# Optimization experiments

Measured on AMD Instinct MI355X. Metric: run time of the kernel, lower is better.

## Reference

```python
import jax, jax.numpy as jnp
import numpy as np
import math

C = 1.0
IN_FEATURES = 512
SCALE = 1.0 / math.sqrt(IN_FEATURES)  # 1/sqrt(input_size) * lr_mul, lr_mul=1
LR_MUL = 1.0
GAIN = math.sqrt(2.0)
EPS = 1e-5       # clamp epsilon used by hyptorch-style pmath
PROJ_EPS = 1e-3  # boundary epsilon for project()


def _norm(x):
    return jnp.linalg.norm(x, axis=-1, keepdims=True)


def _artanh(x):
    return jnp.arctanh(jnp.clip(x, -1.0 + EPS, 1.0 - EPS))


def _project(x, c):
    sqrt_c = c ** 0.5
    norm = jnp.maximum(_norm(x), EPS)
    maxnorm = (1.0 - PROJ_EPS) / sqrt_c
    return jnp.where(norm > maxnorm, x / norm * maxnorm, x)


def _expmap0(u, c):
    sqrt_c = c ** 0.5
    u_norm = jnp.maximum(_norm(u), EPS)
    return jnp.tanh(sqrt_c * u_norm) * u / (sqrt_c * u_norm)


def _mobius_add(x, y, c):
    x2 = jnp.sum(x * x, axis=-1, keepdims=True)
    y2 = jnp.sum(y * y, axis=-1, keepdims=True)
    xy = jnp.sum(x * y, axis=-1, keepdims=True)
    num = (1.0 + 2.0 * c * xy + c * y2) * x + (1.0 - c * x2) * y
    denom = 1.0 + 2.0 * c * xy + c * c * x2 * y2
    return num / (denom + EPS)


def _mobius_matvec(m, x, c):
    # m: [out, in], x: [N, in]
    sqrt_c = c ** 0.5
    x_norm = jnp.maximum(_norm(x), EPS)
    mx = x @ m.T  # [N, out]
    mx_norm = jnp.maximum(_norm(mx), EPS)
    res = jnp.tanh(mx_norm / x_norm * _artanh(sqrt_c * x_norm)) * mx / (mx_norm * sqrt_c)
    zero_row = jnp.all(mx == 0, axis=-1, keepdims=True)
    return jnp.where(zero_row, jnp.zeros_like(res), res)


def _mobius_scalar_mult(x, r, c):
    sqrt_c = c ** 0.5
    x_norm = jnp.maximum(_norm(x), EPS)
    return jnp.tanh(r * _artanh(sqrt_c * x_norm)) * x / (x_norm * sqrt_c)


def setup_inputs() -> dict:
    key = jax.random.key(0)
    k1, k2, k3 = jax.random.split(key, 3)
    N, D_IN, D_OUT = 131072, 512, 512
    # scale x so points lie well inside the unit Poincare ball (norm ~ 0.45)
    x = jax.random.normal(k1, (N, D_IN), dtype=jnp.float32) * 0.02
    weight = jax.random.normal(k2, (D_OUT, D_IN), dtype=jnp.float32)
    bias = jax.random.normal(k3, (D_OUT,), dtype=jnp.float32) * 0.01
    return {"x": x, "weight": weight, "bias": bias}


def reference(x, weight, bias):
    c = C
    mv = _mobius_matvec(weight * SCALE, x, c)
    b = _expmap0(bias * LR_MUL, c)
    out = _project(_mobius_add(mv, b[None, :], c), c)
    out = jax.nn.leaky_relu(out, 0.2)
    out = _mobius_scalar_mult(out, GAIN, c)
    return out
```

## Files before the change

kernel.cpp:

```cpp
#include <hip/hip_runtime.h>
#include <math.h>

#define EPSV 1e-5f
#define SCALE_W 0.0441941738241592f
#define GAIN_R 1.4142135623730951f

typedef __attribute__((ext_vector_type(8))) short bf16x8;
typedef __attribute__((ext_vector_type(4))) float f32x4;

static __device__ __forceinline__ unsigned short f2bf(float f) {
  union { float f; unsigned int u; } v; v.f = f;
  unsigned int r = v.u + 0x7FFFu + ((v.u >> 16) & 1u);
  return (unsigned short)(r >> 16);
}

#define LBAR() do {                                          \
  asm volatile("s_waitcnt lgkmcnt(0)" ::: "memory");         \
  __builtin_amdgcn_sched_barrier(0);                         \
  __builtin_amdgcn_s_barrier();                              \
  __builtin_amdgcn_sched_barrier(0);                         \
  asm volatile("" ::: "memory");                             \
} while (0)

__global__ void bias_expmap_k(const float* __restrict__ bias, float* __restrict__ bexp,
                              float* __restrict__ y2out) {
  __shared__ float part[8];
  int t = threadIdx.x;
  float bv = bias[t];
  float s = bv * bv;
  s += __shfl_xor(s, 1);  s += __shfl_xor(s, 2);  s += __shfl_xor(s, 4);
  s += __shfl_xor(s, 8);  s += __shfl_xor(s, 16); s += __shfl_xor(s, 32);
  if ((t & 63) == 0) part[t >> 6] = s;
  __syncthreads();
  float tot = 0.f;
#pragma unroll
  for (int i = 0; i < 8; ++i) tot += part[i];
  float un = fmaxf(sqrtf(tot), EPSV);
  float th = tanhf(un);
  bexp[t] = th * bv / un;
  if (t == 0) *y2out = th * th;
}

__global__ void pack_weight_k(const float* __restrict__ w, unsigned short* __restrict__ wsB) {
  int e = blockIdx.x * 256 + threadIdx.x;
  int o = e >> 9;
  int k = e & 511;
  int ks = k >> 5, kk = k & 31;
  int lgr = kk >> 3, j = kk & 7;
  int colhi = o >> 4, l15 = o & 15;
  int dst = ((ks * 32 + colhi) * 64 + lgr * 16 + l15) * 8 + j;
  wsB[dst] = f2bf(w[e] * SCALE_W);
}

#define RB 80
#define KSROW 5120
#define BUFSZ 20480
#define SC_OFF 40960
#define SMEMSZ 43776

__global__ __launch_bounds__(256, 2)
void hyp_main_k(const float* __restrict__ x, const unsigned short* __restrict__ wsB,
                const float* __restrict__ bexp, const float* __restrict__ y2p,
                float* __restrict__ out, int tilesPerBlk) {
  extern __shared__ char smem[];
  const int tid  = threadIdx.x;
  const int lane = tid & 63;
  const int wave = tid >> 6;
  const int l15  = lane & 15;
  const int lgr  = lane >> 4;
  const int srow = tid >> 2;
  const int sq   = tid & 3;

  float* xn2 = (float*)(smem + SC_OFF);
  float* pS2 = (float*)(smem + SC_OFF + 256);
  float* pSB = (float*)(smem + SC_OFF + 1280);
  float* g12 = (float*)(smem + SC_OFF + 2304);

  const char* ard0 = smem + l15 * RB + lgr * 16;
  const char* brd  = (const char*)wsB + ((size_t)(wave * 8) * 64 + lane) * 16;
  char* awr0 = smem + sq * KSROW + srow * RB;

  f32x4 acc[4][8];
#pragma unroll
  for (int mf = 0; mf < 4; ++mf)
#pragma unroll
    for (int nf = 0; nf < 8; ++nf) acc[mf][nf] = f32x4{0.f, 0.f, 0.f, 0.f};

  const long base = (long)blockIdx.x * tilesPerBlk;
  const int nss = 4 * tilesPerBlk;
  float xss = 0.f;
  f32x4 st[8];

  {
    const float* p = x + (size_t)(base * 64 + srow) * 512 + sq * 32;
#pragma unroll
    for (int i = 0; i < 8; ++i) st[i] = *(const f32x4*)(p + i * 4);
#pragma unroll
    for (int i = 0; i < 8; ++i) {
      f32x4 v = st[i];
      xss += v[0] * v[0] + v[1] * v[1] + v[2] * v[2] + v[3] * v[3];
      uint2 pk;
      pk.x = (unsigned int)f2bf(v[0]) | ((unsigned int)f2bf(v[1]) << 16);
      pk.y = (unsigned int)f2bf(v[2]) | ((unsigned int)f2bf(v[3]) << 16);
      *(uint2*)(awr0 + i * 8) = pk;
    }
  }
  LBAR();

  for (int s = 0; s < nss; ++s) {
    const int q = s & 3;
    const int buf = s & 1;

    if (s + 1 < nss) {
      const int sp = s + 1;
      const float* p = x + (size_t)((base + (sp >> 2)) * 64 + srow) * 512 + (sp & 3) * 128 + sq * 32;
#pragma unroll
      for (int i = 0; i < 8; ++i) st[i] = *(const f32x4*)(p + i * 4);
    }

#pragma unroll
    for (int ksl = 0; ksl < 4; ++ksl) {
      const int gks = q * 4 + ksl;
      bf16x8 xf[4], wf[8];
#pragma unroll
      for (int mf = 0; mf < 4; ++mf)
        xf[mf] = *(const bf16x8*)(ard0 + buf * BUFSZ + ksl * KSROW + mf * 1280);
#pragma unroll
      for (int nf = 0; nf < 8; ++nf)
        wf[nf] = *(const bf16x8*)(brd + (size_t)gks * 32768 + nf * 1024);
#pragma unroll
      for (int mf = 0; mf < 4; ++mf)
#pragma unroll
        for (int nf = 0; nf < 8; ++nf)
          acc[mf][nf] = __builtin_amdgcn_mfma_f32_16x16x32_bf16(wf[nf], xf[mf], acc[mf][nf], 0, 0, 0);
    }

    if (q == 3) {
      const long tile = base + (s >> 2);

      float xs = xss;
      xs += __shfl_xor(xs, 1); xs += __shfl_xor(xs, 2);
      if (sq == 0) xn2[srow] = xs;
      xss = 0.f;

      f32x4 bvv[8];
#pragma unroll
      for (int nf = 0; nf < 8; ++nf)
        bvv[nf] = *(const f32x4*)(bexp + wave * 128 + nf * 16 + lgr * 4);

      float s2[4], sb[4];
#pragma unroll
      for (int mf = 0; mf < 4; ++mf) {
        s2[mf] = 0.f; sb[mf] = 0.f;
#pragma unroll
        for (int nf = 0; nf < 8; ++nf)
#pragma unroll
          for (int j = 0; j < 4; ++j) {
            float v = acc[mf][nf][j];
            s2[mf] += v * v;
            sb[mf] += v * bvv[nf][j];
          }
        s2[mf] += __shfl_xor(s2[mf], 16); s2[mf] += __shfl_xor(s2[mf], 32);
        sb[mf] += __shfl_xor(sb[mf], 16); sb[mf] += __shfl_xor(sb[mf], 32);
      }
      if (lane < 16) {
#pragma unroll
        for (int mf = 0; mf < 4; ++mf) {
          pS2[(mf * 16 + l15) * 4 + wave] = s2[mf];
          pSB[(mf * 16 + l15) * 4 + wave] = sb[mf];
        }
      }
      LBAR();

      if (tid < 64) {
        int r = tid;
        float S2 = 0.f, SB = 0.f;
#pragma unroll
        for (int i = 0; i < 4; ++i) { S2 += pS2[r * 4 + i]; SB += pSB[r * 4 + i]; }
        float y2 = *y2p;
        float xn  = fmaxf(sqrtf(xn2[r]), EPSV);
        float mxn = fmaxf(sqrtf(S2), EPSV);
        float f = tanhf((mxn / xn) * atanhf(fminf(xn, 1.f - EPSV))) / mxn;
        float xy = f * SB;
        float x2 = f * f * S2;
        float den = 1.f + 2.f * xy + x2 * y2 + EPSV;
        float g1 = (1.f + 2.f * xy + y2) * f / den;
        float g2 = (1.f - x2) / den;
        float n1sq = g1 * g1 * S2 + 2.f * g1 * g2 * SB + g2 * g2 * y2;
        float n1 = fmaxf(sqrtf(fmaxf(n1sq, 0.f)), EPSV);
        if (n1 > 0.999f) { float sc = 0.999f / n1; g1 *= sc; g2 *= sc; }
        g12[r * 2] = g1; g12[r * 2 + 1] = g2;
      }
      LBAR();

      float n2p[4];
#pragma unroll
      for (int mf = 0; mf < 4; ++mf) {
        float g1 = g12[(mf * 16 + l15) * 2], g2 = g12[(mf * 16 + l15) * 2 + 1];
        n2p[mf] = 0.f;
#pragma unroll
        for (int nf = 0; nf < 8; ++nf)
#pragma unroll
          for (int j = 0; j < 4; ++j) {
            float v = g1 * acc[mf][nf][j] + g2 * bvv[nf][j];
            v = v > 0.f ? v : 0.2f * v;
            acc[mf][nf][j] = v;
            n2p[mf] += v * v;
          }
        n2p[mf] += __shfl_xor(n2p[mf], 16); n2p[mf] += __shfl_xor(n2p[mf], 32);
      }
      if (lane < 16) {
#pragma unroll
        for (int mf = 0; mf < 4; ++mf) pS2[(mf * 16 + l15) * 4 + wave] = n2p[mf];
      }
      LBAR();

      if (tid < 64) {
        int r = tid;
        float sn = 0.f;
#pragma unroll
        for (int i = 0; i < 4; ++i) sn += pS2[r * 4 + i];
        float n2 = fmaxf(sqrtf(sn), EPSV);
        xn2[r] = tanhf(GAIN_R * atanhf(fminf(n2, 1.f - EPSV))) / n2;
      }
      LBAR();

#pragma unroll
      for (int mf = 0; mf < 4; ++mf) {
        float tm = xn2[mf * 16 + l15];
#pragma unroll
        for (int nf = 0; nf < 8; ++nf) {
          f32x4 o = acc[mf][nf];
          o[0] *= tm; o[1] *= tm; o[2] *= tm; o[3] *= tm;
          *(f32x4*)(out + (size_t)(tile * 64 + mf * 16 + l15) * 512 +
                    wave * 128 + nf * 16 + lgr * 4) = o;
          acc[mf][nf] = f32x4{0.f, 0.f, 0.f, 0.f};
        }
      }
    }

    if (s + 1 < nss) {
      char* awr = awr0 + ((s + 1) & 1) * BUFSZ;
#pragma unroll
      for (int i = 0; i < 8; ++i) {
        f32x4 v = st[i];
        xss += v[0] * v[0] + v[1] * v[1] + v[2] * v[2] + v[3] * v[3];
        uint2 pk;
        pk.x = (unsigned int)f2bf(v[0]) | ((unsigned int)f2bf(v[1]) << 16);
        pk.y = (unsigned int)f2bf(v[2]) | ((unsigned int)f2bf(v[3]) << 16);
        *(uint2*)(awr + i * 8) = pk;
      }
    }
    LBAR();
  }
}

extern "C" void kernel_launch(void* const* d_in, const int* in_sizes, int n_in,
                              void* d_out, int out_size, void* d_ws, size_t ws_size,
                              hipStream_t stream) {
  const float* x    = (const float*)d_in[0];
  const float* w    = (const float*)d_in[1];
  const float* bias = (const float*)d_in[2];
  float* out = (float*)d_out;

  unsigned short* wsB = (unsigned short*)d_ws;
  float* bexp = (float*)((char*)d_ws + 524288);
  float* y2p  = (float*)((char*)d_ws + 524288 + 2048);

  bias_expmap_k<<<dim3(1), dim3(512), 0, stream>>>(bias, bexp, y2p);
  pack_weight_k<<<dim3(1024), dim3(256), 0, stream>>>(w, wsB);

  const int nrows  = in_sizes[0] / 512;
  const int ntiles = nrows / 64;
  const int nblk   = 512;
  const int tpb    = ntiles / nblk;
  hyp_main_k<<<dim3(nblk), dim3(256), SMEMSZ, stream>>>(x, wsB, bexp, y2p, out, tpb);
}
```

Before: 177.7 us.

## Stream weights through LDS via global_load_lds with deeper x prefetch and 8 waves

Restructures the main GEMM loop to process one 32-wide K-slice per iteration. Weight slices are staged into double-buffered LDS with direct global-to-LDS loads, replacing per-wave global weight reads. The x operand is prefetched two slices ahead into a 4-slot LDS ring. Blocks grow to 512 threads (8 waves, each owning 64 output columns), the grid is halved, and bias values are hoisted out of the epilogue. The intent is better latency hiding and less redundant weight traffic, at the cost of more barriers per K step, higher LDS usage, and fragile vmcnt-based wait accounting.

```diff
diff --git a/kernel.cpp b/kernel.cpp
--- a/kernel.cpp
+++ b/kernel.cpp
@@ -13,13 +13,21 @@
   unsigned int r = v.u + 0x7FFFu + ((v.u >> 16) & 1u);
   return (unsigned short)(r >> 16);
 }
+
+#define GLD_LDS16(gsrc, ldst)                                                                      \
+  __builtin_amdgcn_global_load_lds((const __attribute__((address_space(1))) unsigned int*)(gsrc),  \
+                                   (__attribute__((address_space(3))) unsigned int*)(ldst), 16, 0, 0)
 
 #define LBAR() do {                                          \
   asm volatile("s_waitcnt lgkmcnt(0)" ::: "memory");         \
   __builtin_amdgcn_sched_barrier(0);                         \
   __builtin_amdgcn_s_barrier();                              \
   __builtin_amdgcn_sched_barrier(0);                         \
-  asm volatile("" ::: "memory");                             \
+} while (0)
+
+#define VMW5() do {                                          \
+  asm volatile("s_waitcnt vmcnt(5)" ::: "memory");           \
+  __builtin_amdgcn_sched_barrier(0);                         \
 } while (0)
 
 __global__ void bias_expmap_k(const float* __restrict__ bias, float* __restrict__ bexp,
@@ -52,13 +60,12 @@
   wsB[dst] = f2bf(w[e] * SCALE_W);
 }
 
-#define RB 80
-#define KSROW 5120
-#define BUFSZ 20480
-#define SC_OFF 40960
-#define SMEMSZ 43776
-
-__global__ __launch_bounds__(256, 2)
+#define ASLOT 4608
+#define BOFF_L 18432
+#define SCR 83968
+#define SMEMSZ 88832
+
+__global__ __launch_bounds__(512, 2)
 void hyp_main_k(const float* __restrict__ x, const unsigned short* __restrict__ wsB,
                 const float* __restrict__ bexp, const float* __restrict__ y2p,
                 float* __restrict__ out, int tilesPerBlk) {
@@ -68,92 +75,99 @@
   const int wave = tid >> 6;
   const int l15  = lane & 15;
   const int lgr  = lane >> 4;
-  const int srow = tid >> 2;
-  const int sq   = tid & 3;
-
-  float* xn2 = (float*)(smem + SC_OFF);
-  float* pS2 = (float*)(smem + SC_OFF + 256);
-  float* pSB = (float*)(smem + SC_OFF + 1280);
-  float* g12 = (float*)(smem + SC_OFF + 2304);
-
-  const char* ard0 = smem + l15 * RB + lgr * 16;
-  const char* brd  = (const char*)wsB + ((size_t)(wave * 8) * 64 + lane) * 16;
-  char* awr0 = smem + sq * KSROW + srow * RB;
-
-  f32x4 acc[4][8];
+  const int arow = tid >> 3;
+  const int ag   = tid & 7;
+
+  float* xn2 = (float*)(smem + SCR);
+  float* pS2 = (float*)(smem + SCR + 256);
+  float* pSB = (float*)(smem + SCR + 2304);
+  float* g12 = (float*)(smem + SCR + 4352);
+
+  f32x4 bvv[4];
+#pragma unroll
+  for (int nf = 0; nf < 4; ++nf)
+    bvv[nf] = *(const f32x4*)(bexp + wave * 64 + nf * 16 + lgr * 4);
+  float y2v = *y2p;
+
+  f32x4 acc[4][4];
 #pragma unroll
   for (int mf = 0; mf < 4; ++mf)
 #pragma unroll
-    for (int nf = 0; nf < 8; ++nf) acc[mf][nf] = f32x4{0.f, 0.f, 0.f, 0.f};
-
-  const long base = (long)blockIdx.x * tilesPerBlk;
-  const int nss = 4 * tilesPerBlk;
+    for (int nf = 0; nf < 4; ++nf) acc[mf][nf] = f32x4{0.f, 0.f, 0.f, 0.f};
+
+  const long tile0 = (long)blockIdx.x * tilesPerBlk;
+  const int U = tilesPerBlk * 16;
+  const float* xbase = x + (size_t)(tile0 * 64 + arow) * 512 + ag * 4;
+
   float xss = 0.f;
-  f32x4 st[8];
+  f32x4 Lprev, Lcur;
 
   {
-    const float* p = x + (size_t)(base * 64 + srow) * 512 + sq * 32;
-#pragma unroll
-    for (int i = 0; i < 8; ++i) st[i] = *(const f32x4*)(p + i * 4);
-#pragma unroll
-    for (int i = 0; i < 8; ++i) {
-      f32x4 v = st[i];
+    f32x4 a0 = *(const f32x4*)(xbase);
+    f32x4 a1 = *(const f32x4*)(xbase + 32);
+#pragma unroll
+    for (int i = 0; i < 2; ++i) {
+      f32x4 v = (i == 0) ? a0 : a1;
       xss += v[0] * v[0] + v[1] * v[1] + v[2] * v[2] + v[3] * v[3];
       uint2 pk;
       pk.x = (unsigned int)f2bf(v[0]) | ((unsigned int)f2bf(v[1]) << 16);
       pk.y = (unsigned int)f2bf(v[2]) | ((unsigned int)f2bf(v[3]) << 16);
-      *(uint2*)(awr0 + i * 8) = pk;
+      *(uint2*)(smem + i * ASLOT + arow * 72 + ag * 8) = pk;
     }
   }
+#pragma unroll
+  for (int r = 0; r < 4; ++r)
+    GLD_LDS16((const char*)wsB + r * 8192 + wave * 1024 + lane * 16,
+              smem + BOFF_L + r * 8192 + wave * 1024);
   LBAR();
 
-  for (int s = 0; s < nss; ++s) {
-    const int q = s & 3;
-    const int buf = s & 1;
-
-    if (s + 1 < nss) {
-      const int sp = s + 1;
-      const float* p = x + (size_t)((base + (sp >> 2)) * 64 + srow) * 512 + (sp & 3) * 128 + sq * 32;
-#pragma unroll
-      for (int i = 0; i < 8; ++i) st[i] = *(const f32x4*)(p + i * 4);
-    }
-
-#pragma unroll
-    for (int ksl = 0; ksl < 4; ++ksl) {
-      const int gks = q * 4 + ksl;
-      bf16x8 xf[4], wf[8];
+#pragma unroll 1
+  for (int u = 0; u < U; ++u) {
+    {
+      int gu = u + 2; if (gu >= U) gu = 0;
+      Lcur = *(const f32x4*)(xbase + (size_t)(gu >> 4) * 32768 + (gu & 15) * 32);
+    }
+    {
+      const char* bsrc = (const char*)wsB + (size_t)((u + 1) & 15) * 32768;
+      char* bdst = smem + BOFF_L + ((u + 1) & 1) * 32768;
+#pragma unroll
+      for (int r = 0; r < 4; ++r)
+        GLD_LDS16(bsrc + r * 8192 + wave * 1024 + lane * 16, bdst + r * 8192 + wave * 1024);
+    }
+    VMW5();
+    LBAR();
+
+    {
+      const char* as = smem + (u & 3) * ASLOT + l15 * 72 + lgr * 16;
+      const char* bb = smem + BOFF_L + (u & 1) * 32768 + (size_t)(wave * 4) * 1024 + lane * 16;
+      bf16x8 xf[4], wf[4];
+#pragma unroll
+      for (int mf = 0; mf < 4; ++mf) xf[mf] = *(const bf16x8*)(as + mf * (16 * 72));
+#pragma unroll
+      for (int nf = 0; nf < 4; ++nf) wf[nf] = *(const bf16x8*)(bb + nf * 1024);
+      __builtin_amdgcn_s_setprio(1);
 #pragma unroll
       for (int mf = 0; mf < 4; ++mf)
-        xf[mf] = *(const bf16x8*)(ard0 + buf * BUFSZ + ksl * KSROW + mf * 1280);
-#pragma unroll
-      for (int nf = 0; nf < 8; ++nf)
-        wf[nf] = *(const bf16x8*)(brd + (size_t)gks * 32768 + nf * 1024);
-#pragma unroll
-      for (int mf = 0; mf < 4; ++mf)
-#pragma unroll
-        for (int nf = 0; nf < 8; ++nf)
+#pragma unroll
+        for (int nf = 0; nf < 4; ++nf)
           acc[mf][nf] = __builtin_amdgcn_mfma_f32_16x16x32_bf16(wf[nf], xf[mf], acc[mf][nf], 0, 0, 0);
-    }
-
-    if (q == 3) {
-      const long tile = base + (s >> 2);
+      __builtin_amdgcn_s_setprio(0);
+    }
+
+    if ((u & 15) == 15) {
+      const long trow = (tile0 + (u >> 4)) * 64;
 
       float xs = xss;
-      xs += __shfl_xor(xs, 1); xs += __shfl_xor(xs, 2);
-      if (sq == 0) xn2[srow] = xs;
+      xs += __shfl_xor(xs, 1); xs += __shfl_xor(xs, 2); xs += __shfl_xor(xs, 4);
+      if ((lane & 7) == 0) xn2[wave * 8 + (lane >> 3)] = xs;
       xss = 0.f;
-
-      f32x4 bvv[8];
-#pragma unroll
-      for (int nf = 0; nf < 8; ++nf)
-        bvv[nf] = *(const f32x4*)(bexp + wave * 128 + nf * 16 + lgr * 4);
 
       float s2[4], sb[4];
 #pragma unroll
       for (int mf = 0; mf < 4; ++mf) {
         s2[mf] = 0.f; sb[mf] = 0.f;
 #pragma unroll
-        for (int nf = 0; nf < 8; ++nf)
+        for (int nf = 0; nf < 4; ++nf)
 #pragma unroll
           for (int j = 0; j < 4; ++j) {
             float v = acc[mf][nf][j];
@@ -166,8 +180,8 @@
       if (lane < 16) {
 #pragma unroll
         for (int mf = 0; mf < 4; ++mf) {
-          pS2[(mf * 16 + l15) * 4 + wave] = s2[mf];
-          pSB[(mf * 16 + l15) * 4 + wave] = sb[mf];
+          pS2[(mf * 16 + l15) * 8 + wave] = s2[mf];
+          pSB[(mf * 16 + l15) * 8 + wave] = sb[mf];
         }
       }
       LBAR();
@@ -176,17 +190,16 @@
         int r = tid;
         float S2 = 0.f, SB = 0.f;
 #pragma unroll
-        for (int i = 0; i < 4; ++i) { S2 += pS2[r * 4 + i]; SB += pSB[r * 4 + i]; }
-        float y2 = *y2p;
+        for (int i = 0; i < 8; ++i) { S2 += pS2[r * 8 + i]; SB += pSB[r * 8 + i]; }
         float xn  = fmaxf(sqrtf(xn2[r]), EPSV);
         float mxn = fmaxf(sqrtf(S2), EPSV);
         float f = tanhf((mxn / xn) * atanhf(fminf(xn, 1.f - EPSV))) / mxn;
         float xy = f * SB;
         float x2 = f * f * S2;
-        float den = 1.f + 2.f * xy + x2 * y2 + EPSV;
-        float g1 = (1.f + 2.f * xy + y2) * f / den;
+        float den = 1.f + 2.f * xy + x2 * y2v + EPSV;
+        float g1 = (1.f + 2.f * xy + y2v) * f / den;
         float g2 = (1.f - x2) / den;
-        float n1sq = g1 * g1 * S2 + 2.f * g1 * g2 * SB + g2 * g2 * y2;
+        float n1sq = g1 * g1 * S2 + 2.f * g1 * g2 * SB + g2 * g2 * y2v;
         float n1 = fmaxf(sqrtf(fmaxf(n1sq, 0.f)), EPSV);
         if (n1 > 0.999f) { float sc = 0.999f / n1; g1 *= sc; g2 *= sc; }
         g12[r * 2] = g1; g12[r * 2 + 1] = g2;
@@ -199,7 +212,7 @@
         float g1 = g12[(mf * 16 + l15) * 2], g2 = g12[(mf * 16 + l15) * 2 + 1];
         n2p[mf] = 0.f;
 #pragma unroll
-        for (int nf = 0; nf < 8; ++nf)
+        for (int nf = 0; nf < 4; ++nf)
 #pragma unroll
           for (int j = 0; j < 4; ++j) {
             float v = g1 * acc[mf][nf][j] + g2 * bvv[nf][j];
@@ -211,7 +224,7 @@
       }
       if (lane < 16) {
 #pragma unroll
-        for (int mf = 0; mf < 4; ++mf) pS2[(mf * 16 + l15) * 4 + wave] = n2p[mf];
+        for (int mf = 0; mf < 4; ++mf) pS2[(mf * 16 + l15) * 8 + wave] = n2p[mf];
       }
       LBAR();
 
@@ -219,7 +232,7 @@
         int r = tid;
         float sn = 0.f;
 #pragma unroll
-        for (int i = 0; i < 4; ++i) sn += pS2[r * 4 + i];
+        for (int i = 0; i < 8; ++i) sn += pS2[r * 8 + i];
         float n2 = fmaxf(sqrtf(sn), EPSV);
         xn2[r] = tanhf(GAIN_R * atanhf(fminf(n2, 1.f - EPSV))) / n2;
       }
@@ -229,28 +242,25 @@
       for (int mf = 0; mf < 4; ++mf) {
         float tm = xn2[mf * 16 + l15];
 #pragma unroll
-        for (int nf = 0; nf < 8; ++nf) {
+        for (int nf = 0; nf < 4; ++nf) {
           f32x4 o = acc[mf][nf];
           o[0] *= tm; o[1] *= tm; o[2] *= tm; o[3] *= tm;
-          *(f32x4*)(out + (size_t)(tile * 64 + mf * 16 + l15) * 512 +
-                    wave * 128 + nf * 16 + lgr * 4) = o;
+          *(f32x4*)(out + (size_t)(trow + mf * 16 + l15) * 512 +
+                    wave * 64 + nf * 16 + lgr * 4) = o;
           acc[mf][nf] = f32x4{0.f, 0.f, 0.f, 0.f};
         }
       }
     }
 
-    if (s + 1 < nss) {
-      char* awr = awr0 + ((s + 1) & 1) * BUFSZ;
-#pragma unroll
-      for (int i = 0; i < 8; ++i) {
-        f32x4 v = st[i];
-        xss += v[0] * v[0] + v[1] * v[1] + v[2] * v[2] + v[3] * v[3];
-        uint2 pk;
-        pk.x = (unsigned int)f2bf(v[0]) | ((unsigned int)f2bf(v[1]) << 16);
-        pk.y = (unsigned int)f2bf(v[2]) | ((unsigned int)f2bf(v[3]) << 16);
-        *(uint2*)(awr + i * 8) = pk;
-      }
-    }
+    if (u > 0) {
+      f32x4 v = Lprev;
+      xss += v[0] * v[0] + v[1] * v[1] + v[2] * v[2] + v[3] * v[3];
+      uint2 pk;
+      pk.x = (unsigned int)f2bf(v[0]) | ((unsigned int)f2bf(v[1]) << 16);
+      pk.y = (unsigned int)f2bf(v[2]) | ((unsigned int)f2bf(v[3]) << 16);
+      *(uint2*)(smem + ((u + 1) & 3) * ASLOT + arow * 72 + ag * 8) = pk;
+    }
+    Lprev = Lcur;
     LBAR();
   }
 }
@@ -272,7 +282,7 @@
 
   const int nrows  = in_sizes[0] / 512;
   const int ntiles = nrows / 64;
-  const int nblk   = 512;
+  const int nblk   = 256;
   const int tpb    = ntiles / nblk;
-  hyp_main_k<<<dim3(nblk), dim3(256), SMEMSZ, stream>>>(x, wsB, bexp, y2p, out, tpb);
-}
+  hyp_main_k<<<dim3(nblk), dim3(512), SMEMSZ, stream>>>(x, wsB, bexp, y2p, out, tpb);
+}
```

Result: slower. 264.4 us (+48.8%).

## Stream weight slices into LDS via async global_load_lds with per-k-step double buffering

Applied to the files above, without the earlier changes.

The main loop is restructured so each iteration handles one 32-wide k-slice instead of four. The weight slice is loaded asynchronously into double-buffered LDS with global_load_lds, where before each wave read weights straight from global memory. The next x slice is prefetched into registers, and explicit vmcnt waits control how far loads may run ahead. Bias and y2 are also cached in LDS and MFMA issue gets a raised priority. In exchange LDS use nearly doubles, which may limit occupancy, and there are now sixteen barriers per tile instead of four.

```diff
diff --git a/kernel.cpp b/kernel.cpp
--- a/kernel.cpp
+++ b/kernel.cpp
@@ -7,19 +7,28 @@
 
 typedef __attribute__((ext_vector_type(8))) short bf16x8;
 typedef __attribute__((ext_vector_type(4))) float f32x4;
+typedef __attribute__((ext_vector_type(4))) unsigned int u32x4;
 
 static __device__ __forceinline__ unsigned short f2bf(float f) {
   union { float f; unsigned int u; } v; v.f = f;
   unsigned int r = v.u + 0x7FFFu + ((v.u >> 16) & 1u);
   return (unsigned short)(r >> 16);
 }
+
+#define GLD_LDS16(gsrc, ldst)                                                                      \
+  __builtin_amdgcn_global_load_lds((const __attribute__((address_space(1))) unsigned int*)(gsrc),  \
+                                   (__attribute__((address_space(3))) unsigned int*)(ldst), 16, 0, 0)
 
 #define LBAR() do {                                          \
   asm volatile("s_waitcnt lgkmcnt(0)" ::: "memory");         \
   __builtin_amdgcn_sched_barrier(0);                         \
   __builtin_amdgcn_s_barrier();                              \
   __builtin_amdgcn_sched_barrier(0);                         \
-  asm volatile("" ::: "memory");                             \
+} while (0)
+
+#define VMCNT(N) do {                                        \
+  asm volatile("s_waitcnt vmcnt(" #N ")" ::: "memory");      \
+  __builtin_amdgcn_sched_barrier(0);                         \
 } while (0)
 
 __global__ void bias_expmap_k(const float* __restrict__ bias, float* __restrict__ bexp,
@@ -53,10 +62,11 @@
 }
 
 #define RB 80
-#define KSROW 5120
-#define BUFSZ 20480
-#define SC_OFF 40960
-#define SMEMSZ 43776
+#define ABUF 5120
+#define BOFF 10240
+#define BBUF 32768
+#define SCR 75776
+#define SMEMSZ 80896
 
 __global__ __launch_bounds__(256, 2)
 void hyp_main_k(const float* __restrict__ x, const unsigned short* __restrict__ wsB,
@@ -71,14 +81,12 @@
   const int srow = tid >> 2;
   const int sq   = tid & 3;
 
-  float* xn2 = (float*)(smem + SC_OFF);
-  float* pS2 = (float*)(smem + SC_OFF + 256);
-  float* pSB = (float*)(smem + SC_OFF + 1280);
-  float* g12 = (float*)(smem + SC_OFF + 2304);
-
-  const char* ard0 = smem + l15 * RB + lgr * 16;
-  const char* brd  = (const char*)wsB + ((size_t)(wave * 8) * 64 + lane) * 16;
-  char* awr0 = smem + sq * KSROW + srow * RB;
+  float* xn2      = (float*)(smem + SCR);
+  float* pS2      = (float*)(smem + SCR + 256);
+  float* pSB      = (float*)(smem + SCR + 1280);
+  float* g12      = (float*)(smem + SCR + 2304);
+  float* bexp_lds = (float*)(smem + SCR + 2816);
+  float* y2l      = (float*)(smem + SCR + 4864);
 
   f32x4 acc[4][8];
 #pragma unroll
@@ -87,56 +95,70 @@
     for (int nf = 0; nf < 8; ++nf) acc[mf][nf] = f32x4{0.f, 0.f, 0.f, 0.f};
 
   const long base = (long)blockIdx.x * tilesPerBlk;
-  const int nss = 4 * tilesPerBlk;
+  const int U = tilesPerBlk * 16;
   float xss = 0.f;
-  f32x4 st[8];
+  f32x4 stA, stB;
 
   {
-    const float* p = x + (size_t)(base * 64 + srow) * 512 + sq * 32;
-#pragma unroll
-    for (int i = 0; i < 8; ++i) st[i] = *(const f32x4*)(p + i * 4);
-#pragma unroll
-    for (int i = 0; i < 8; ++i) {
-      f32x4 v = st[i];
-      xss += v[0] * v[0] + v[1] * v[1] + v[2] * v[2] + v[3] * v[3];
-      uint2 pk;
-      pk.x = (unsigned int)f2bf(v[0]) | ((unsigned int)f2bf(v[1]) << 16);
-      pk.y = (unsigned int)f2bf(v[2]) | ((unsigned int)f2bf(v[3]) << 16);
-      *(uint2*)(awr0 + i * 8) = pk;
-    }
+    float2 bc = *(const float2*)(bexp + tid * 2);
+    *(float2*)(bexp_lds + tid * 2) = bc;
+    if (tid == 0) *y2l = *y2p;
+    const float* p = x + (size_t)(base * 64 + srow) * 512 + sq * 8;
+    f32x4 a = *(const f32x4*)p;
+    f32x4 b = *(const f32x4*)(p + 4);
+    xss += a[0]*a[0] + a[1]*a[1] + a[2]*a[2] + a[3]*a[3];
+    xss += b[0]*b[0] + b[1]*b[1] + b[2]*b[2] + b[3]*b[3];
+    u32x4 pk;
+    pk[0] = (unsigned int)f2bf(a[0]) | ((unsigned int)f2bf(a[1]) << 16);
+    pk[1] = (unsigned int)f2bf(a[2]) | ((unsigned int)f2bf(a[3]) << 16);
+    pk[2] = (unsigned int)f2bf(b[0]) | ((unsigned int)f2bf(b[1]) << 16);
+    pk[3] = (unsigned int)f2bf(b[2]) | ((unsigned int)f2bf(b[3]) << 16);
+    *(u32x4*)(smem + srow * RB + sq * 16) = pk;
+#pragma unroll
+    for (int i = 0; i < 8; ++i)
+      GLD_LDS16((const char*)wsB + (wave * 8 + i) * 1024 + lane * 16,
+                smem + BOFF + (wave * 8 + i) * 1024);
   }
   LBAR();
 
-  for (int s = 0; s < nss; ++s) {
-    const int q = s & 3;
-    const int buf = s & 1;
-
-    if (s + 1 < nss) {
-      const int sp = s + 1;
-      const float* p = x + (size_t)((base + (sp >> 2)) * 64 + srow) * 512 + (sp & 3) * 128 + sq * 32;
-#pragma unroll
-      for (int i = 0; i < 8; ++i) st[i] = *(const f32x4*)(p + i * 4);
-    }
-
-#pragma unroll
-    for (int ksl = 0; ksl < 4; ++ksl) {
-      const int gks = q * 4 + ksl;
+#pragma unroll 1
+  for (int t = 0; t < U; ++t) {
+    const int cur = t & 1, nxt = cur ^ 1;
+
+    {
+      const int gu = (t + 1 < U) ? t + 1 : U - 1;
+      const float* p = x + (size_t)((base + (gu >> 4)) * 64 + srow) * 512 + (gu & 15) * 32 + sq * 8;
+      stA = *(const f32x4*)p;
+      stB = *(const f32x4*)(p + 4);
+    }
+    {
+      const char* bs = (const char*)wsB + (size_t)((t + 1) & 15) * 32768;
+      char* bd = smem + BOFF + nxt * BBUF;
+#pragma unroll
+      for (int i = 0; i < 8; ++i)
+        GLD_LDS16(bs + (wave * 8 + i) * 1024 + lane * 16, bd + (wave * 8 + i) * 1024);
+    }
+    if (t > 0 && (t & 15) == 0) { VMCNT(42); } else { VMCNT(10); }
+
+    {
+      const char* ab = smem + cur * ABUF + l15 * RB + lgr * 16;
+      const char* bb = smem + BOFF + cur * BBUF + (wave * 8) * 1024 + lane * 16;
       bf16x8 xf[4], wf[8];
 #pragma unroll
-      for (int mf = 0; mf < 4; ++mf)
-        xf[mf] = *(const bf16x8*)(ard0 + buf * BUFSZ + ksl * KSROW + mf * 1280);
-#pragma unroll
-      for (int nf = 0; nf < 8; ++nf)
-        wf[nf] = *(const bf16x8*)(brd + (size_t)gks * 32768 + nf * 1024);
+      for (int mf = 0; mf < 4; ++mf) xf[mf] = *(const bf16x8*)(ab + mf * (16 * RB));
+#pragma unroll
+      for (int nf = 0; nf < 8; ++nf) wf[nf] = *(const bf16x8*)(bb + nf * 1024);
+      __builtin_amdgcn_s_setprio(1);
 #pragma unroll
       for (int mf = 0; mf < 4; ++mf)
 #pragma unroll
         for (int nf = 0; nf < 8; ++nf)
           acc[mf][nf] = __builtin_amdgcn_mfma_f32_16x16x32_bf16(wf[nf], xf[mf], acc[mf][nf], 0, 0, 0);
-    }
-
-    if (q == 3) {
-      const long tile = base + (s >> 2);
+      __builtin_amdgcn_s_setprio(0);
+    }
+
+    if ((t & 15) == 15) {
+      const long trow = (base + (t >> 4)) * 64;
 
       float xs = xss;
       xs += __shfl_xor(xs, 1); xs += __shfl_xor(xs, 2);
@@ -146,7 +168,8 @@
       f32x4 bvv[8];
 #pragma unroll
       for (int nf = 0; nf < 8; ++nf)
-        bvv[nf] = *(const f32x4*)(bexp + wave * 128 + nf * 16 + lgr * 4);
+        bvv[nf] = *(const f32x4*)(bexp_lds + wave * 128 + nf * 16 + lgr * 4);
+      const float y2 = *y2l;
 
       float s2[4], sb[4];
 #pragma unroll
@@ -177,16 +200,16 @@
         float S2 = 0.f, SB = 0.f;
 #pragma unroll
         for (int i = 0; i < 4; ++i) { S2 += pS2[r * 4 + i]; SB += pSB[r * 4 + i]; }
-        float y2 = *y2p;
+        float y2s = *y2l;
         float xn  = fmaxf(sqrtf(xn2[r]), EPSV);
         float mxn = fmaxf(sqrtf(S2), EPSV);
         float f = tanhf((mxn / xn) * atanhf(fminf(xn, 1.f - EPSV))) / mxn;
         float xy = f * SB;
         float x2 = f * f * S2;
-        float den = 1.f + 2.f * xy + x2 * y2 + EPSV;
-        float g1 = (1.f + 2.f * xy + y2) * f / den;
+        float den = 1.f + 2.f * xy + x2 * y2s + EPSV;
+        float g1 = (1.f + 2.f * xy + y2s) * f / den;
         float g2 = (1.f - x2) / den;
-        float n1sq = g1 * g1 * S2 + 2.f * g1 * g2 * SB + g2 * g2 * y2;
+        float n1sq = g1 * g1 * S2 + 2.f * g1 * g2 * SB + g2 * g2 * y2s;
         float n1 = fmaxf(sqrtf(fmaxf(n1sq, 0.f)), EPSV);
         if (n1 > 0.999f) { float sc = 0.999f / n1; g1 *= sc; g2 *= sc; }
         g12[r * 2] = g1; g12[r * 2 + 1] = g2;
@@ -232,24 +255,25 @@
         for (int nf = 0; nf < 8; ++nf) {
           f32x4 o = acc[mf][nf];
           o[0] *= tm; o[1] *= tm; o[2] *= tm; o[3] *= tm;
-          *(f32x4*)(out + (size_t)(tile * 64 + mf * 16 + l15) * 512 +
+          *(f32x4*)(out + (size_t)(trow + mf * 16 + l15) * 512 +
                     wave * 128 + nf * 16 + lgr * 4) = o;
           acc[mf][nf] = f32x4{0.f, 0.f, 0.f, 0.f};
         }
       }
     }
 
-    if (s + 1 < nss) {
-      char* awr = awr0 + ((s + 1) & 1) * BUFSZ;
-#pragma unroll
-      for (int i = 0; i < 8; ++i) {
-        f32x4 v = st[i];
-        xss += v[0] * v[0] + v[1] * v[1] + v[2] * v[2] + v[3] * v[3];
-        uint2 pk;
-        pk.x = (unsigned int)f2bf(v[0]) | ((unsigned int)f2bf(v[1]) << 16);
-        pk.y = (unsigned int)f2bf(v[2]) | ((unsigned int)f2bf(v[3]) << 16);
-        *(uint2*)(awr + i * 8) = pk;
-      }
+    if ((t & 15) == 15) { VMCNT(40); } else { VMCNT(8); }
+
+    {
+      f32x4 a = stA, b = stB;
+      xss += a[0]*a[0] + a[1]*a[1] + a[2]*a[2] + a[3]*a[3];
+      xss += b[0]*b[0] + b[1]*b[1] + b[2]*b[2] + b[3]*b[3];
+      u32x4 pk;
+      pk[0] = (unsigned int)f2bf(a[0]) | ((unsigned int)f2bf(a[1]) << 16);
+      pk[1] = (unsigned int)f2bf(a[2]) | ((unsigned int)f2bf(a[3]) << 16);
+      pk[2] = (unsigned int)f2bf(b[0]) | ((unsigned int)f2bf(b[1]) << 16);
+      pk[3] = (unsigned int)f2bf(b[2]) | ((unsigned int)f2bf(b[3]) << 16);
+      *(u32x4*)(smem + nxt * ABUF + srow * RB + sq * 16) = pk;
     }
     LBAR();
   }
```

New measurement: 177.2 us. No clear change (-0.3%).
